# Kernel tuning notes

Measured on AMD Instinct MI355X. Metric: run time of the kernel, lower is better.

Reference implementation:

```python
import jax, jax.numpy as jnp
import numpy as np

DIM = 128
NUM_LAYERS = 5
EPS = 1e-5


def setup_inputs() -> dict:
    key = jax.random.key(0)
    ks = jax.random.split(key, 16)
    N, E, D = 50000, 640000, DIM
    x = jax.random.uniform(ks[0], (N, 3), dtype=jnp.float32)
    edge_index = jax.random.randint(ks[1], (2, E), 0, N, dtype=jnp.int64)
    norm = jax.random.uniform(ks[2], (E,), dtype=jnp.float32)
    s3 = 1.0 / np.sqrt(3.0)
    sd = 1.0 / np.sqrt(D)
    return {
        "x": x,
        "edge_index": edge_index,
        "norm": norm,
        "W_enc": jax.random.uniform(ks[3], (D, 3), jnp.float32, -s3, s3),
        "bn_e_gamma": jnp.ones((D,), jnp.float32),
        "bn_e_beta": jnp.zeros((D,), jnp.float32),
        "W_ih": jax.random.uniform(ks[4], (3 * D, D), jnp.float32, -sd, sd),
        "W_hh": jax.random.uniform(ks[5], (3 * D, D), jnp.float32, -sd, sd),
        "b_ih": jax.random.uniform(ks[6], (3 * D,), jnp.float32, -sd, sd),
        "b_hh": jax.random.uniform(ks[7], (3 * D,), jnp.float32, -sd, sd),
        "W_dec": jax.random.uniform(ks[8], (D // 2, D), jnp.float32, -sd, sd),
        "bn_d_gamma": jnp.ones((D // 2,), jnp.float32),
        "bn_d_beta": jnp.zeros((D // 2,), jnp.float32),
        "W_dec2": jax.random.uniform(ks[9], (1, D // 2), jnp.float32, -sd * np.sqrt(2.0), sd * np.sqrt(2.0)),
    }


def batchnorm(h, gamma, beta):
    # training-mode BatchNorm1d: biased batch stats over the node dimension
    mu = jnp.mean(h, axis=0)
    var = jnp.var(h, axis=0)
    return (h - mu) * jax.lax.rsqrt(var + EPS) * gamma + beta


def gru_cell(inp, hid, W_ih, W_hh, b_ih, b_hh):
    gi = inp @ W_ih.T + b_ih  # [N, 3D]
    gh = hid @ W_hh.T + b_hh
    D = hid.shape[1]
    i_r, i_z, i_n = gi[:, :D], gi[:, D:2 * D], gi[:, 2 * D:]
    h_r, h_z, h_n = gh[:, :D], gh[:, D:2 * D], gh[:, 2 * D:]
    r = jax.nn.sigmoid(i_r + h_r)
    z = jax.nn.sigmoid(i_z + h_z)
    n = jnp.tanh(i_n + r * h_n)
    return (1.0 - z) * n + z * hid


def reference(x, edge_index, norm, W_enc, bn_e_gamma, bn_e_beta, W_ih, W_hh, b_ih, b_hh, W_dec, bn_d_gamma, bn_d_beta, W_dec2):
    N = x.shape[0]
    src, dst = edge_index[0], edge_index[1]
    # encode
    h = jax.nn.relu(batchnorm(x @ W_enc.T, bn_e_gamma, bn_e_beta))  # [N, D]
    h_sum = h
    prev_h = h
    for _ in range(NUM_LAYERS):
        # neighborhood aggregation: scatter-add of norm-weighted source features
        msg = norm[:, None] * prev_h[src]  # [E, D]
        h_agg = jax.ops.segment_sum(msg, dst, num_segments=N)  # [N, D]
        h_sum = h_sum + h_agg
        prev_h = gru_cell(h_agg, prev_h, W_ih, W_hh, b_ih, b_hh)
    z = h_sum / (NUM_LAYERS + 1)  # mean over stacked h_list
    # decode
    y = jax.nn.relu(batchnorm(z @ W_dec.T, bn_d_gamma, bn_d_beta))
    y = y @ W_dec2.T  # [N, 1]
    return y.reshape(-1)
```

## Files before the change

kernel.cpp:

```cpp
#include <hip/hip_runtime.h>

#define DD 128

typedef _Float16 f16x8 __attribute__((ext_vector_type(8)));
typedef unsigned short u16x8 __attribute__((ext_vector_type(8)));
typedef unsigned short u16x4 __attribute__((ext_vector_type(4)));
typedef float f32x4 __attribute__((ext_vector_type(4)));

__device__ __forceinline__ float sigmoidf_(float v){ return 1.f/(1.f+__expf(-v)); }
__device__ __forceinline__ float tanhf_(float v){
  float e2 = __expf(2.f*v);
  return 1.f - 2.f/(e2 + 1.f);
}
__device__ __forceinline__ float h2f(unsigned short u){
  _Float16 h; __builtin_memcpy(&h, &u, 2); return (float)h;
}
__device__ __forceinline__ unsigned short f2h(float v){
  _Float16 h = (_Float16)v; unsigned short u; __builtin_memcpy(&u, &h, 2); return u;
}

#define PREP_B 416
__global__ void __launch_bounds__(256) k_pre1(
        const float* __restrict__ W_ih, const float* __restrict__ W_hh,
        const float* __restrict__ W_dec, const float* __restrict__ x,
        const float* __restrict__ W_enc, const int* __restrict__ dst,
        unsigned short* __restrict__ Wih_h, unsigned short* __restrict__ Whh_h,
        unsigned short* __restrict__ Wd_h, unsigned short* __restrict__ h0,
        float* __restrict__ stats, int* __restrict__ counts, int N, int E){
  const int tid = threadIdx.x;
  const int gb = blockIdx.x;
  const int TOT = 384*128;
  if (gb < PREP_B){
    int idx = gb*256 + tid;
    if (idx < 2*TOT){
      const float* W = (idx < TOT) ? W_ih : W_hh;
      unsigned short* D = (idx < TOT) ? Wih_h : Whh_h;
      int fi = (idx < TOT) ? idx : idx - TOT;
      int t = fi & 7;
      int l = (fi >> 3) & 63;
      int ks = (fi >> 9) & 3;
      int nt = fi >> 11;
      int fg = nt / 3, gate = nt % 3;
      int j = gate*128 + fg*16 + (l & 15);
      int k = ks*32 + ((l >> 4) & 3)*8 + t;
      D[fi] = f2h(W[j*128 + k]);
    } else if (idx < 2*TOT + 64*128){
      int fi2 = idx - 2*TOT;
      int t  = fi2 & 7;
      int l  = (fi2 >> 3) & 63;
      int ks = (fi2 >> 9) & 3;
      int jt = fi2 >> 11;
      int j = jt*16 + (l & 15);
      int k = ks*32 + ((l >> 4) & 3)*8 + t;
      Wd_h[fi2] = f2h(W_dec[j*128 + k]);
    }
  } else if (gb < PREP_B + 256){
    const int b = gb - PREP_B;
    const int f = tid & 127;
    const int sub = tid >> 7;
    const float w0 = W_enc[f*3], w1 = W_enc[f*3+1], w2 = W_enc[f*3+2];
    const int chunk = (N + 255) / 256;
    const int n0 = b * chunk;
    const int n1 = (n0 + chunk < N) ? (n0 + chunk) : N;
    float s = 0.f, q = 0.f;
    for (int n = n0 + sub; n < n1; n += 2){
      float x0 = x[n*3], x1 = x[n*3+1], x2 = x[n*3+2];
      float h = x0*w0 + x1*w1 + x2*w2;
      unsigned short hu = f2h(h);
      float hq = h2f(hu);
      h0[(size_t)n*DD + f] = hu;
      s += hq; q += hq*hq;
    }
    atomicAdd(&stats[f], s);
    atomicAdd(&stats[DD+f], q);
  } else {
    int e = (gb - PREP_B - 256)*256 + tid;
    if (e < E) atomicAdd(&counts[dst[e]], 1);
  }
}

__global__ void __launch_bounds__(256) k_scan_part(const int* __restrict__ counts,
                                                   int* __restrict__ partials, int N){
  int i = blockIdx.x*256 + threadIdx.x;
  int v = (i < N) ? counts[i] : 0;
  #pragma unroll
  for (int off = 32; off > 0; off >>= 1) v += __shfl_down(v, off, 64);
  __shared__ int red[4];
  if ((threadIdx.x & 63) == 0) red[threadIdx.x >> 6] = v;
  __syncthreads();
  if (threadIdx.x == 0) partials[blockIdx.x] = red[0]+red[1]+red[2]+red[3];
}

__global__ void __launch_bounds__(256) k_scan_mid(int* __restrict__ partials, int P,
                                                  int* __restrict__ offsets, int N){
  __shared__ int lds[4];
  __shared__ int carry_s;
  const int lane = threadIdx.x & 63, wid = threadIdx.x >> 6;
  if (threadIdx.x == 0) carry_s = 0;
  __syncthreads();
  for (int base = 0; base < P; base += 256){
    int i = base + threadIdx.x;
    int v = (i < P) ? partials[i] : 0;
    int orig = v;
    #pragma unroll
    for (int off = 1; off < 64; off <<= 1){
      int u = __shfl_up(v, off, 64);
      if (lane >= off) v += u;
    }
    if (lane == 63) lds[wid] = v;
    __syncthreads();
    if (threadIdx.x == 0){
      int s = carry_s;
      for (int k = 0; k < 4; k++){ int t = lds[k]; lds[k] = s; s += t; }
      carry_s = s;
    }
    __syncthreads();
    int excl = v - orig + lds[wid];
    if (i < P) partials[i] = excl;
    __syncthreads();
  }
  if (threadIdx.x == 0) offsets[N] = carry_s;
}

__global__ void __launch_bounds__(256) k_scan_expand(const int* __restrict__ counts,
        const int* __restrict__ partials, int* __restrict__ offsets,
        int* __restrict__ cursors, int N){
  int i = blockIdx.x*256 + threadIdx.x;
  int v = (i < N) ? counts[i] : 0;
  int orig = v;
  const int lane = threadIdx.x & 63, wid = threadIdx.x >> 6;
  #pragma unroll
  for (int off = 1; off < 64; off <<= 1){
    int u = __shfl_up(v, off, 64);
    if (lane >= off) v += u;
  }
  __shared__ int lds[4];
  if (lane == 63) lds[wid] = v;
  __syncthreads();
  int wbase = 0;
  for (int k = 0; k < wid; k++) wbase += lds[k];
  int excl = partials[blockIdx.x] + wbase + v - orig;
  if (i < N){ offsets[i] = excl; cursors[i] = excl; }
}

__global__ void __launch_bounds__(256) k_pre2(
        const unsigned short* __restrict__ h0, const float* __restrict__ gamma,
        const float* __restrict__ beta, const float* __restrict__ stats,
        unsigned short* __restrict__ ph, unsigned short* __restrict__ hbn,
        const int* __restrict__ src, const int* __restrict__ dst,
        const float* __restrict__ norm, int* __restrict__ cursors,
        int2* __restrict__ csr, int N, int E, int AB){
  const int tid = threadIdx.x;
  if ((int)blockIdx.x < AB){
    int idx = blockIdx.x*256 + tid;
    if (idx >= N*DD) return;
    int f = idx & (DD-1);
    float invN = 1.f / (float)N;
    float mu = stats[f] * invN;
    float var = stats[DD+f] * invN - mu*mu;
    float v = (h2f(h0[idx]) - mu) * rsqrtf(var + 1e-5f) * gamma[f] + beta[f];
    v = fmaxf(v, 0.f);
    unsigned short hv = f2h(v);
    ph[idx] = hv;
    hbn[idx] = hv;
  } else {
    int e = ((int)blockIdx.x - AB)*256 + tid;
    if (e >= E) return;
    int p = atomicAdd(&cursors[dst[e]], 1);
    union { float f; int i; } c; c.f = norm[e];
    csr[p] = make_int2(src[e], c.i);
  }
}

__global__ void __launch_bounds__(512, 4) k_layer(
        const unsigned short* __restrict__ phc,
        unsigned short* __restrict__ phn,
        unsigned short* __restrict__ agg_out,
        const int* __restrict__ offsets, const int2* __restrict__ csr,
        const unsigned short* __restrict__ Wih_h, const unsigned short* __restrict__ Whh_h,
        const float* __restrict__ b_ih, const float* __restrict__ b_hh, int N){
  __shared__ unsigned short s_a[32*DD];
  const int tid = threadIdx.x;
  const int n0 = blockIdx.x * 32;

  {
    const int m = tid >> 4;
    const int q = tid & 15;
    const int n = n0 + m;
    float acc[8];
    #pragma unroll
    for (int t = 0; t < 8; t++) acc[t] = 0.f;
    if (n < N){
      const int s0 = offsets[n], s1 = offsets[n+1];
      int i = s0;
      for (; i + 8 <= s1; i += 8){
        int2 ed[8]; u16x8 R[8];
        #pragma unroll
        for (int u = 0; u < 8; u++) ed[u] = csr[i+u];
        #pragma unroll
        for (int u = 0; u < 8; u++) R[u] = *(const u16x8*)(phc + (size_t)ed[u].x*DD + q*8);
        #pragma unroll
        for (int u = 0; u < 8; u++){
          union { int i; float f; } c; c.i = ed[u].y;
          #pragma unroll
          for (int t = 0; t < 8; t++)
            acc[t] = fmaf(c.f, h2f((unsigned short)R[u][t]), acc[t]);
        }
      }
      if (i + 4 <= s1){
        int2 ed[4]; u16x8 R[4];
        #pragma unroll
        for (int u = 0; u < 4; u++) ed[u] = csr[i+u];
        #pragma unroll
        for (int u = 0; u < 4; u++) R[u] = *(const u16x8*)(phc + (size_t)ed[u].x*DD + q*8);
        #pragma unroll
        for (int u = 0; u < 4; u++){
          union { int i; float f; } c; c.i = ed[u].y;
          #pragma unroll
          for (int t = 0; t < 8; t++)
            acc[t] = fmaf(c.f, h2f((unsigned short)R[u][t]), acc[t]);
        }
        i += 4;
      }
      for (; i < s1; i++){
        int2 ed = csr[i];
        union { int i; float f; } c; c.i = ed.y;
        u16x8 R = *(const u16x8*)(phc + (size_t)ed.x*DD + q*8);
        #pragma unroll
        for (int t = 0; t < 8; t++)
          acc[t] = fmaf(c.f, h2f((unsigned short)R[t]), acc[t]);
      }
    }
    u16x8 vh;
    #pragma unroll
    for (int t = 0; t < 8; t++) vh[t] = f2h(acc[t]);
    if (n < N)
      *(u16x8*)(agg_out + (size_t)n*DD + q*8) = vh;
    const int cc = q ^ (m & 7);
    *(u16x8*)(s_a + m*DD + cc*8) = vh;
  }
  __syncthreads();

  const int w = tid >> 6, l = tid & 63, ar = l & 15, aq = l >> 4;
  int r0 = n0 + ar;      if (r0 >= N) r0 = N-1;
  int r1 = n0 + 16 + ar; if (r1 >= N) r1 = N-1;
  const size_t p0 = (size_t)r0*DD + aq*8;
  const size_t p1 = (size_t)r1*DD + aq*8;
  const int sw = ar & 7;

  f32x4 acc_i[2][3], acc_h[2][3];
  #pragma unroll
  for (int ta = 0; ta < 2; ta++)
    #pragma unroll
    for (int t = 0; t < 3; t++){
      acc_i[ta][t] = (f32x4){0.f,0.f,0.f,0.f};
      acc_h[ta][t] = (f32x4){0.f,0.f,0.f,0.f};
    }

  #pragma unroll
  for (int ks = 0; ks < 4; ks++){
    const int c = (ks*4 + aq) ^ sw;
    f16x8 ih0 = *(const f16x8*)(s_a + ar*DD       + c*8);
    f16x8 ih1 = *(const f16x8*)(s_a + (16+ar)*DD  + c*8);
    f16x8 hh0 = *(const f16x8*)(phc + p0 + ks*32);
    f16x8 hh1 = *(const f16x8*)(phc + p1 + ks*32);
    #pragma unroll
    for (int t = 0; t < 3; t++){
      size_t bo = ((size_t)((w*3 + t)*4 + ks)*64 + l)*8;
      f16x8 bih = *(const f16x8*)(Wih_h + bo);
      f16x8 bhh = *(const f16x8*)(Whh_h + bo);
      acc_i[0][t] = __builtin_amdgcn_mfma_f32_16x16x32_f16(ih0, bih, acc_i[0][t], 0, 0, 0);
      acc_i[1][t] = __builtin_amdgcn_mfma_f32_16x16x32_f16(ih1, bih, acc_i[1][t], 0, 0, 0);
      acc_h[0][t] = __builtin_amdgcn_mfma_f32_16x16x32_f16(hh0, bhh, acc_h[0][t], 0, 0, 0);
      acc_h[1][t] = __builtin_amdgcn_mfma_f32_16x16x32_f16(hh1, bhh, acc_h[1][t], 0, 0, 0);
    }
  }

  const int f = w*16 + ar;
  const float bir = b_ih[f], biz = b_ih[128+f], bin_ = b_ih[256+f];
  const float bhr = b_hh[f], bhz = b_hh[128+f], bhn = b_hh[256+f];
  float hv[2][4];
  #pragma unroll
  for (int ta = 0; ta < 2; ta++){
    #pragma unroll
    for (int r = 0; r < 4; r++){
      int n = n0 + ta*16 + aq*4 + r;
      if (n < N){
        float sir = acc_i[ta][0][r] + bir, shr = acc_h[ta][0][r] + bhr;
        float siz = acc_i[ta][1][r] + biz, shz = acc_h[ta][1][r] + bhz;
        float sin_ = acc_i[ta][2][r] + bin_, shn = acc_h[ta][2][r] + bhn;
        float rr = sigmoidf_(sir + shr);
        float zz = sigmoidf_(siz + shz);
        float nn = tanhf_(sin_ + rr*shn);
        float hp = h2f(phc[(size_t)n*DD + f]);
        hv[ta][r] = (1.f - zz)*nn + zz*hp;
      }
    }
  }
  __syncthreads();
  #pragma unroll
  for (int ta = 0; ta < 2; ta++){
    #pragma unroll
    for (int r = 0; r < 4; r++){
      int m2 = ta*16 + aq*4 + r;
      if (n0 + m2 < N) s_a[m2*DD + f] = f2h(hv[ta][r]);
    }
  }
  __syncthreads();
  {
    int idx = tid * 8;
    int n = n0 + (idx >> 7);
    if (n < N)
      *(u16x8*)(phn + (size_t)n0*DD + idx) = *(const u16x8*)(s_a + idx);
  }
}

__global__ void __launch_bounds__(256, 8) k_dec1(const unsigned short* __restrict__ hbn,
        const unsigned short* __restrict__ aggs, size_t NF,
        const unsigned short* __restrict__ ph5,
        const int* __restrict__ offsets, const int2* __restrict__ csr,
        const unsigned short* __restrict__ Wd_h, unsigned short* __restrict__ y1,
        float* __restrict__ stats_d, int N){
  __shared__ unsigned short zs[16*DD];
  __shared__ unsigned short stage[16*64];
  const int tid = threadIdx.x;
  const int n0 = blockIdx.x * 16;

  {
    const int m = tid >> 4;
    const int q = tid & 15;
    const int n = n0 + m;
    float acc[8];
    #pragma unroll
    for (int t = 0; t < 8; t++) acc[t] = 0.f;
    if (n < N){
      size_t o = (size_t)n*DD + q*8;
      u16x8 hb = *(const u16x8*)(hbn + o);
      #pragma unroll
      for (int t = 0; t < 8; t++) acc[t] = h2f(hb[t]);
      #pragma unroll
      for (int l = 0; l < 4; l++){
        u16x8 ag = *(const u16x8*)(aggs + l*NF + o);
        #pragma unroll
        for (int t = 0; t < 8; t++) acc[t] += h2f(ag[t]);
      }
      const int s0 = offsets[n], s1 = offsets[n+1];
      int i = s0;
      for (; i + 8 <= s1; i += 8){
        int2 ed[8]; u16x8 R[8];
        #pragma unroll
        for (int u = 0; u < 8; u++) ed[u] = csr[i+u];
        #pragma unroll
        for (int u = 0; u < 8; u++) R[u] = *(const u16x8*)(ph5 + (size_t)ed[u].x*DD + q*8);
        #pragma unroll
        for (int u = 0; u < 8; u++){
          union { int i; float f; } c; c.i = ed[u].y;
          #pragma unroll
          for (int t = 0; t < 8; t++)
            acc[t] = fmaf(c.f, h2f((unsigned short)R[u][t]), acc[t]);
        }
      }
      if (i + 4 <= s1){
        int2 ed[4]; u16x8 R[4];
        #pragma unroll
        for (int u = 0; u < 4; u++) ed[u] = csr[i+u];
        #pragma unroll
        for (int u = 0; u < 4; u++) R[u] = *(const u16x8*)(ph5 + (size_t)ed[u].x*DD + q*8);
        #pragma unroll
        for (int u = 0; u < 4; u++){
          union { int i; float f; } c; c.i = ed[u].y;
          #pragma unroll
          for (int t = 0; t < 8; t++)
            acc[t] = fmaf(c.f, h2f((unsigned short)R[u][t]), acc[t]);
        }
        i += 4;
      }
      for (; i < s1; i++){
        int2 ed = csr[i];
        union { int i; float f; } c; c.i = ed.y;
        u16x8 R = *(const u16x8*)(ph5 + (size_t)ed.x*DD + q*8);
        #pragma unroll
        for (int t = 0; t < 8; t++)
          acc[t] = fmaf(c.f, h2f((unsigned short)R[t]), acc[t]);
      }
    }
    u16x8 vh;
    #pragma unroll
    for (int t = 0; t < 8; t++) vh[t] = f2h(acc[t] * (1.f/6.f));
    const int cc = q ^ (m & 7);
    *(u16x8*)(zs + m*DD + cc*8) = vh;
  }
  __syncthreads();

  const int w = tid >> 6, l = tid & 63, ar = l & 15, aq = l >> 4;
  const int sw = ar & 7;
  f32x4 acc = (f32x4){0.f,0.f,0.f,0.f};
  #pragma unroll
  for (int ks = 0; ks < 4; ks++){
    const int c = (ks*4 + aq) ^ sw;
    f16x8 a = *(const f16x8*)(zs + ar*DD + c*8);
    f16x8 b = *(const f16x8*)(Wd_h + ((size_t)(w*4 + ks)*64 + l)*8);
    acc = __builtin_amdgcn_mfma_f32_16x16x32_f16(a, b, acc, 0, 0, 0);
  }
  float s = 0.f, q2 = 0.f;
  #pragma unroll
  for (int r = 0; r < 4; r++){
    int n = n0 + aq*4 + r;
    float v = acc[r];
    if (n < N){
      stage[(aq*4 + r)*64 + w*16 + ar] = f2h(v);
      s += v; q2 += v*v;
    }
  }
  s  += __shfl_xor(s, 16, 64);  s  += __shfl_xor(s, 32, 64);
  q2 += __shfl_xor(q2, 16, 64); q2 += __shfl_xor(q2, 32, 64);
  if (aq == 0){
    float* st = stats_d + (size_t)(blockIdx.x & 7)*128;
    atomicAdd(&st[w*16 + ar], s);
    atomicAdd(&st[64 + w*16 + ar], q2);
  }
  __syncthreads();
  {
    int idx = tid * 4;
    int n = n0 + (idx >> 6);
    if (n < N)
      *(u16x4*)(y1 + (size_t)n0*64 + idx) = *(const u16x4*)(stage + idx);
  }
}

__global__ void __launch_bounds__(256) k_dec2(const unsigned short* __restrict__ y1,
        const float* __restrict__ gamma, const float* __restrict__ beta,
        const float* __restrict__ W_dec2, const float* __restrict__ stats_d,
        float* __restrict__ out, int N){
  const int j = threadIdx.x & 63;
  const int g = threadIdx.x >> 6;
  const int n = blockIdx.x*4 + g;
  if (n >= N) return;
  float ssum = 0.f, qsum = 0.f;
  #pragma unroll
  for (int c = 0; c < 8; c++){
    ssum += stats_d[c*128 + j];
    qsum += stats_d[c*128 + 64 + j];
  }
  float invN = 1.f / (float)N;
  float mu = ssum * invN;
  float var = qsum * invN - mu*mu;
  float v = (h2f(y1[(size_t)n*64 + j]) - mu) * rsqrtf(var + 1e-5f) * gamma[j] + beta[j];
  v = fmaxf(v, 0.f) * W_dec2[j];
  for (int off = 32; off > 0; off >>= 1) v += __shfl_down(v, off, 64);
  if (j == 0) out[n] = v;
}

extern "C" void kernel_launch(void* const* d_in, const int* in_sizes, int n_in,
                              void* d_out, int out_size, void* d_ws, size_t ws_size,
                              hipStream_t stream) {
  const int N = in_sizes[0] / 3;
  const int E = in_sizes[1] / 2;
  const int P = (N + 255) / 256;
  const int HIST_B = (E + 255) / 256;
  const int AB = (N*DD + 255) / 256;

  const float* x     = (const float*)d_in[0];
  const int*   ei    = (const int*)d_in[1];
  const int*   src   = ei;
  const int*   dst   = ei + E;
  const float* norm  = (const float*)d_in[2];
  const float* W_enc = (const float*)d_in[3];
  const float* g_e   = (const float*)d_in[4];
  const float* b_e   = (const float*)d_in[5];
  const float* W_ih  = (const float*)d_in[6];
  const float* W_hh  = (const float*)d_in[7];
  const float* b_ih  = (const float*)d_in[8];
  const float* b_hh  = (const float*)d_in[9];
  const float* W_dec = (const float*)d_in[10];
  const float* g_d   = (const float*)d_in[11];
  const float* b_d   = (const float*)d_in[12];
  const float* W_dec2= (const float*)d_in[13];
  float* out = (float*)d_out;

  float* ws = (float*)d_ws;
  const size_t NF = (size_t)N * DD;
  float* scr    = ws;
  unsigned short* h0h = (unsigned short*)scr;
  unsigned short* y1h = (unsigned short*)scr;
  float* stats  = scr + NF;
  float* Wt_dec = stats + 1280;
  unsigned short* Wd_h  = (unsigned short*)Wt_dec;
  unsigned short* Wih_h = (unsigned short*)(Wt_dec + 64*128);
  unsigned short* Whh_h = Wih_h + 384*128;
  unsigned short* ph_A  = Whh_h + 384*128;
  unsigned short* ph_B  = ph_A + NF;
  unsigned short* hbn   = ph_B + NF;
  unsigned short* aggs  = hbn + NF;
  int*   counts  = (int*)(aggs + 4*NF);
  int*   offsets = counts + N;
  int*   cursors = offsets + N + 1;
  int*   partials= cursors + N;
  int2*  csr     = (int2*)(partials + P);

  hipMemsetAsync(stats, 0, 1280*sizeof(float), stream);
  hipMemsetAsync(counts, 0, (size_t)N*sizeof(int), stream);

  k_pre1<<<PREP_B + 256 + HIST_B, 256, 0, stream>>>(
      W_ih, W_hh, W_dec, x, W_enc, dst,
      Wih_h, Whh_h, Wd_h, h0h, stats, counts, N, E);
  k_scan_part<<<P, 256, 0, stream>>>(counts, partials, N);
  k_scan_mid<<<1, 256, 0, stream>>>(partials, P, offsets, N);
  k_scan_expand<<<P, 256, 0, stream>>>(counts, partials, offsets, cursors, N);
  k_pre2<<<AB + HIST_B, 256, 0, stream>>>(
      h0h, g_e, b_e, stats, ph_A, hbn,
      src, dst, norm, cursors, csr, N, E, AB);

  unsigned short* phh_c = ph_A;
  unsigned short* phh_n = ph_B;
  for (int l = 0; l < 4; l++){
    k_layer<<<(N + 31)/32, 512, 0, stream>>>(phh_c, phh_n, aggs + (size_t)l*NF,
                                             offsets, csr,
                                             Wih_h, Whh_h, b_ih, b_hh, N);
    unsigned short* t = phh_c; phh_c = phh_n; phh_n = t;
  }

  k_dec1<<<(N + 15)/16, 256, 0, stream>>>(hbn, aggs, NF, phh_c, offsets, csr,
                                          Wd_h, y1h, stats + 256, N);
  k_dec2<<<(N + 3)/4, 256, 0, stream>>>(y1h, g_d, b_d, W_dec2, stats + 256, out, N);
}
```

Before: 521.2 us.

## Halve k_layer block to 256 threads, each gathering two nodes interleaved

k_layer now runs 256 threads per 32-node block instead of 512. Each thread gathers two destination rows at once, interleaving their CSR edge loads so more memory requests are in flight, then finishes each row with a shared drain helper. Each wave now computes two 16-feature GRU groups in sequence and writes the new hidden state straight to global memory, dropping the LDS staging pass and two barriers. The cost is fewer threads per block, more registers per thread, and scattered 2-byte global stores in place of coalesced 16-byte ones.

```diff
diff --git a/kernel.cpp b/kernel.cpp
--- a/kernel.cpp
+++ b/kernel.cpp
@@ -17,6 +17,47 @@
 }
 __device__ __forceinline__ unsigned short f2h(float v){
   _Float16 h = (_Float16)v; unsigned short u; __builtin_memcpy(&u, &h, 2); return u;
+}
+
+__device__ __forceinline__ void gather_drain(const unsigned short* __restrict__ phc,
+        const int2* __restrict__ csr, int i, int e, int q, float* acc){
+  for (; i + 8 <= e; i += 8){
+    int2 ed[8]; u16x8 R[8];
+    #pragma unroll
+    for (int u = 0; u < 8; u++) ed[u] = csr[i+u];
+    #pragma unroll
+    for (int u = 0; u < 8; u++) R[u] = *(const u16x8*)(phc + (size_t)ed[u].x*DD + q*8);
+    #pragma unroll
+    for (int u = 0; u < 8; u++){
+      union { int i; float f; } c; c.i = ed[u].y;
+      #pragma unroll
+      for (int t = 0; t < 8; t++)
+        acc[t] = fmaf(c.f, h2f((unsigned short)R[u][t]), acc[t]);
+    }
+  }
+  if (i + 4 <= e){
+    int2 ed[4]; u16x8 R[4];
+    #pragma unroll
+    for (int u = 0; u < 4; u++) ed[u] = csr[i+u];
+    #pragma unroll
+    for (int u = 0; u < 4; u++) R[u] = *(const u16x8*)(phc + (size_t)ed[u].x*DD + q*8);
+    #pragma unroll
+    for (int u = 0; u < 4; u++){
+      union { int i; float f; } c; c.i = ed[u].y;
+      #pragma unroll
+      for (int t = 0; t < 8; t++)
+        acc[t] = fmaf(c.f, h2f((unsigned short)R[u][t]), acc[t]);
+    }
+    i += 4;
+  }
+  for (; i < e; i++){
+    int2 ed = csr[i];
+    union { int i; float f; } c; c.i = ed.y;
+    u16x8 R = *(const u16x8*)(phc + (size_t)ed.x*DD + q*8);
+    #pragma unroll
+    for (int t = 0; t < 8; t++)
+      acc[t] = fmaf(c.f, h2f((unsigned short)R[t]), acc[t]);
+  }
 }
 
 #define PREP_B 416
@@ -172,7 +213,7 @@
   }
 }
 
-__global__ void __launch_bounds__(512, 4) k_layer(
+__global__ void __launch_bounds__(256, 4) k_layer(
         const unsigned short* __restrict__ phc,
         unsigned short* __restrict__ phn,
         unsigned short* __restrict__ agg_out,
@@ -186,58 +227,47 @@
   {
     const int m = tid >> 4;
     const int q = tid & 15;
-    const int n = n0 + m;
-    float acc[8];
-    #pragma unroll
-    for (int t = 0; t < 8; t++) acc[t] = 0.f;
-    if (n < N){
-      const int s0 = offsets[n], s1 = offsets[n+1];
-      int i = s0;
-      for (; i + 8 <= s1; i += 8){
-        int2 ed[8]; u16x8 R[8];
+    const int nA = n0 + m;
+    const int nB = n0 + 16 + m;
+    float aA[8], aB[8];
+    #pragma unroll
+    for (int t = 0; t < 8; t++){ aA[t] = 0.f; aB[t] = 0.f; }
+    int iA = 0, eA = 0, iB = 0, eB = 0;
+    if (nA < N){ iA = offsets[nA]; eA = offsets[nA+1]; }
+    if (nB < N){ iB = offsets[nB]; eB = offsets[nB+1]; }
+
+    while (iA + 4 <= eA && iB + 4 <= eB){
+      int2 edA[4], edB[4];
+      #pragma unroll
+      for (int u = 0; u < 4; u++){ edA[u] = csr[iA+u]; edB[u] = csr[iB+u]; }
+      u16x8 RA[4], RB[4];
+      #pragma unroll
+      for (int u = 0; u < 4; u++){
+        RA[u] = *(const u16x8*)(phc + (size_t)edA[u].x*DD + q*8);
+        RB[u] = *(const u16x8*)(phc + (size_t)edB[u].x*DD + q*8);
+      }
+      #pragma unroll
+      for (int u = 0; u < 4; u++){
+        union { int i; float f; } cA, cB; cA.i = edA[u].y; cB.i = edB[u].y;
         #pragma unroll
-        for (int u = 0; u < 8; u++) ed[u] = csr[i+u];
-        #pragma unroll
-        for (int u = 0; u < 8; u++) R[u] = *(const u16x8*)(phc + (size_t)ed[u].x*DD + q*8);
-        #pragma unroll
-        for (int u = 0; u < 8; u++){
-          union { int i; float f; } c; c.i = ed[u].y;
-          #pragma unroll
-          for (int t = 0; t < 8; t++)
-            acc[t] = fmaf(c.f, h2f((unsigned short)R[u][t]), acc[t]);
+        for (int t = 0; t < 8; t++){
+          aA[t] = fmaf(cA.f, h2f((unsigned short)RA[u][t]), aA[t]);
+          aB[t] = fmaf(cB.f, h2f((unsigned short)RB[u][t]), aB[t]);
         }
       }
-      if (i + 4 <= s1){
-        int2 ed[4]; u16x8 R[4];
-        #pragma unroll
-        for (int u = 0; u < 4; u++) ed[u] = csr[i+u];
-        #pragma unroll
-        for (int u = 0; u < 4; u++) R[u] = *(const u16x8*)(phc + (size_t)ed[u].x*DD + q*8);
-        #pragma unroll
-        for (int u = 0; u < 4; u++){
-          union { int i; float f; } c; c.i = ed[u].y;
-          #pragma unroll
-          for (int t = 0; t < 8; t++)
-            acc[t] = fmaf(c.f, h2f((unsigned short)R[u][t]), acc[t]);
-        }
-        i += 4;
-      }
-      for (; i < s1; i++){
-        int2 ed = csr[i];
-        union { int i; float f; } c; c.i = ed.y;
-        u16x8 R = *(const u16x8*)(phc + (size_t)ed.x*DD + q*8);
-        #pragma unroll
-        for (int t = 0; t < 8; t++)
-          acc[t] = fmaf(c.f, h2f((unsigned short)R[t]), acc[t]);
-      }
-    }
-    u16x8 vh;
-    #pragma unroll
-    for (int t = 0; t < 8; t++) vh[t] = f2h(acc[t]);
-    if (n < N)
-      *(u16x8*)(agg_out + (size_t)n*DD + q*8) = vh;
-    const int cc = q ^ (m & 7);
-    *(u16x8*)(s_a + m*DD + cc*8) = vh;
+      iA += 4; iB += 4;
+    }
+    gather_drain(phc, csr, iA, eA, q, aA);
+    gather_drain(phc, csr, iB, eB, q, aB);
+
+    u16x8 vA, vB;
+    #pragma unroll
+    for (int t = 0; t < 8; t++){ vA[t] = f2h(aA[t]); vB[t] = f2h(aB[t]); }
+    if (nA < N) *(u16x8*)(agg_out + (size_t)nA*DD + q*8) = vA;
+    if (nB < N) *(u16x8*)(agg_out + (size_t)nB*DD + q*8) = vB;
+    const int ccA = q ^ (m & 7);
+    *(u16x8*)(s_a + m*DD + ccA*8) = vA;
+    *(u16x8*)(s_a + (16+m)*DD + ccA*8) = vB;
   }
   __syncthreads();
 
@@ -248,70 +278,58 @@
   const size_t p1 = (size_t)r1*DD + aq*8;
   const int sw = ar & 7;
 
-  f32x4 acc_i[2][3], acc_h[2][3];
-  #pragma unroll
-  for (int ta = 0; ta < 2; ta++)
-    #pragma unroll
-    for (int t = 0; t < 3; t++){
-      acc_i[ta][t] = (f32x4){0.f,0.f,0.f,0.f};
-      acc_h[ta][t] = (f32x4){0.f,0.f,0.f,0.f};
-    }
-
-  #pragma unroll
-  for (int ks = 0; ks < 4; ks++){
-    const int c = (ks*4 + aq) ^ sw;
-    f16x8 ih0 = *(const f16x8*)(s_a + ar*DD       + c*8);
-    f16x8 ih1 = *(const f16x8*)(s_a + (16+ar)*DD  + c*8);
-    f16x8 hh0 = *(const f16x8*)(phc + p0 + ks*32);
-    f16x8 hh1 = *(const f16x8*)(phc + p1 + ks*32);
-    #pragma unroll
-    for (int t = 0; t < 3; t++){
-      size_t bo = ((size_t)((w*3 + t)*4 + ks)*64 + l)*8;
-      f16x8 bih = *(const f16x8*)(Wih_h + bo);
-      f16x8 bhh = *(const f16x8*)(Whh_h + bo);
-      acc_i[0][t] = __builtin_amdgcn_mfma_f32_16x16x32_f16(ih0, bih, acc_i[0][t], 0, 0, 0);
-      acc_i[1][t] = __builtin_amdgcn_mfma_f32_16x16x32_f16(ih1, bih, acc_i[1][t], 0, 0, 0);
-      acc_h[0][t] = __builtin_amdgcn_mfma_f32_16x16x32_f16(hh0, bhh, acc_h[0][t], 0, 0, 0);
-      acc_h[1][t] = __builtin_amdgcn_mfma_f32_16x16x32_f16(hh1, bhh, acc_h[1][t], 0, 0, 0);
-    }
-  }
-
-  const int f = w*16 + ar;
-  const float bir = b_ih[f], biz = b_ih[128+f], bin_ = b_ih[256+f];
-  const float bhr = b_hh[f], bhz = b_hh[128+f], bhn = b_hh[256+f];
-  float hv[2][4];
-  #pragma unroll
-  for (int ta = 0; ta < 2; ta++){
-    #pragma unroll
-    for (int r = 0; r < 4; r++){
-      int n = n0 + ta*16 + aq*4 + r;
-      if (n < N){
-        float sir = acc_i[ta][0][r] + bir, shr = acc_h[ta][0][r] + bhr;
-        float siz = acc_i[ta][1][r] + biz, shz = acc_h[ta][1][r] + bhz;
-        float sin_ = acc_i[ta][2][r] + bin_, shn = acc_h[ta][2][r] + bhn;
-        float rr = sigmoidf_(sir + shr);
-        float zz = sigmoidf_(siz + shz);
-        float nn = tanhf_(sin_ + rr*shn);
-        float hp = h2f(phc[(size_t)n*DD + f]);
-        hv[ta][r] = (1.f - zz)*nn + zz*hp;
+  for (int g = 0; g < 2; g++){
+    const int fg = w*2 + g;
+    f32x4 acc_i[2][3], acc_h[2][3];
+    #pragma unroll
+    for (int ta = 0; ta < 2; ta++)
+      #pragma unroll
+      for (int t = 0; t < 3; t++){
+        acc_i[ta][t] = (f32x4){0.f,0.f,0.f,0.f};
+        acc_h[ta][t] = (f32x4){0.f,0.f,0.f,0.f};
       }
-    }
-  }
-  __syncthreads();
-  #pragma unroll
-  for (int ta = 0; ta < 2; ta++){
-    #pragma unroll
-    for (int r = 0; r < 4; r++){
-      int m2 = ta*16 + aq*4 + r;
-      if (n0 + m2 < N) s_a[m2*DD + f] = f2h(hv[ta][r]);
-    }
-  }
-  __syncthreads();
-  {
-    int idx = tid * 8;
-    int n = n0 + (idx >> 7);
-    if (n < N)
-      *(u16x8*)(phn + (size_t)n0*DD + idx) = *(const u16x8*)(s_a + idx);
+
+    #pragma unroll
+    for (int ks = 0; ks < 4; ks++){
+      const int c = (ks*4 + aq) ^ sw;
+      f16x8 ih0 = *(const f16x8*)(s_a + ar*DD       + c*8);
+      f16x8 ih1 = *(const f16x8*)(s_a + (16+ar)*DD  + c*8);
+      f16x8 hh0 = *(const f16x8*)(phc + p0 + ks*32);
+      f16x8 hh1 = *(const f16x8*)(phc + p1 + ks*32);
+      #pragma unroll
+      for (int t = 0; t < 3; t++){
+        size_t bo = ((size_t)((fg*3 + t)*4 + ks)*64 + l)*8;
+        f16x8 bih = *(const f16x8*)(Wih_h + bo);
+        f16x8 bhh = *(const f16x8*)(Whh_h + bo);
+        acc_i[0][t] = __builtin_amdgcn_mfma_f32_16x16x32_f16(ih0, bih, acc_i[0][t], 0, 0, 0);
+        acc_i[1][t] = __builtin_amdgcn_mfma_f32_16x16x32_f16(ih1, bih, acc_i[1][t], 0, 0, 0);
+        acc_h[0][t] = __builtin_amdgcn_mfma_f32_16x16x32_f16(hh0, bhh, acc_h[0][t], 0, 0, 0);
+        acc_h[1][t] = __builtin_amdgcn_mfma_f32_16x16x32_f16(hh1, bhh, acc_h[1][t], 0, 0, 0);
+      }
+    }
+
+    const int f = fg*16 + ar;
+    const float bir = b_ih[f], biz = b_ih[128+f], bin_ = b_ih[256+f];
+    const float bhr = b_hh[f], bhz = b_hh[128+f], bhn = b_hh[256+f];
+    #pragma unroll
+    for (int ta = 0; ta < 2; ta++){
+      #pragma unroll
+      for (int r = 0; r < 4; r++){
+        int n = n0 + ta*16 + aq*4 + r;
+        if (n < N){
+          float sir = acc_i[ta][0][r] + bir, shr = acc_h[ta][0][r] + bhr;
+          float siz = acc_i[ta][1][r] + biz, shz = acc_h[ta][1][r] + bhz;
+          float sin_ = acc_i[ta][2][r] + bin_, shn = acc_h[ta][2][r] + bhn;
+          float rr = sigmoidf_(sir + shr);
+          float zz = sigmoidf_(siz + shz);
+          float nn = tanhf_(sin_ + rr*shn);
+          size_t o = (size_t)n*DD + f;
+          float hp = h2f(phc[o]);
+          float h = (1.f - zz)*nn + zz*hp;
+          phn[o] = f2h(h);
+        }
+      }
+    }
   }
 }
 
@@ -344,45 +362,7 @@
         #pragma unroll
         for (int t = 0; t < 8; t++) acc[t] += h2f(ag[t]);
       }
-      const int s0 = offsets[n], s1 = offsets[n+1];
-      int i = s0;
-      for (; i + 8 <= s1; i += 8){
-        int2 ed[8]; u16x8 R[8];
-        #pragma unroll
-        for (int u = 0; u < 8; u++) ed[u] = csr[i+u];
-        #pragma unroll
-        for (int u = 0; u < 8; u++) R[u] = *(const u16x8*)(ph5 + (size_t)ed[u].x*DD + q*8);
-        #pragma unroll
-        for (int u = 0; u < 8; u++){
-          union { int i; float f; } c; c.i = ed[u].y;
-          #pragma unroll
-          for (int t = 0; t < 8; t++)
-            acc[t] = fmaf(c.f, h2f((unsigned short)R[u][t]), acc[t]);
-        }
-      }
-      if (i + 4 <= s1){
-        int2 ed[4]; u16x8 R[4];
-        #pragma unroll
-        for (int u = 0; u < 4; u++) ed[u] = csr[i+u];
-        #pragma unroll
-        for (int u = 0; u < 4; u++) R[u] = *(const u16x8*)(ph5 + (size_t)ed[u].x*DD + q*8);
-        #pragma unroll
-        for (int u = 0; u < 4; u++){
-          union { int i; float f; } c; c.i = ed[u].y;
-          #pragma unroll
-          for (int t = 0; t < 8; t++)
-            acc[t] = fmaf(c.f, h2f((unsigned short)R[u][t]), acc[t]);
-        }
-        i += 4;
-      }
-      for (; i < s1; i++){
-        int2 ed = csr[i];
-        union { int i; float f; } c; c.i = ed.y;
-        u16x8 R = *(const u16x8*)(ph5 + (size_t)ed.x*DD + q*8);
-        #pragma unroll
-        for (int t = 0; t < 8; t++)
-          acc[t] = fmaf(c.f, h2f((unsigned short)R[t]), acc[t]);
-      }
+      gather_drain(ph5, csr, offsets[n], offsets[n+1], q, acc);
     }
     u16x8 vh;
     #pragma unroll
@@ -514,7 +494,7 @@
   unsigned short* phh_c = ph_A;
   unsigned short* phh_n = ph_B;
   for (int l = 0; l < 4; l++){
-    k_layer<<<(N + 31)/32, 512, 0, stream>>>(phh_c, phh_n, aggs + (size_t)l*NF,
+    k_layer<<<(N + 31)/32, 256, 0, stream>>>(phh_c, phh_n, aggs + (size_t)l*NF,
                                              offsets, csr,
                                              Wih_h, Whh_h, b_ih, b_hh, N);
     unsigned short* t = phh_c; phh_c = phh_n; phh_n = t;
```

Measured after the change: 477.8 us. -8.3%, faster.
